# Performance work log

Measured on AMD Instinct MI355X. Metric: run time of the kernel, lower is better.

## Reference

```python
import jax, jax.numpy as jnp
import numpy as np

N = 20000      # number of boxes / graph nodes
E = 160000     # random edges (before self-loops)
DIM = 1024     # feature dim (SIA default)


def setup_inputs() -> dict:
    key = jax.random.key(0)
    ks = jax.random.split(key, 12)
    feats = jax.random.normal(ks[0], (N, DIM), dtype=jnp.float32)
    boxes = jax.random.uniform(ks[1], (N, 4), dtype=jnp.float32)
    src = jax.random.randint(ks[2], (E,), 0, N, dtype=jnp.int32)
    dst = jax.random.randint(ks[3], (E,), 0, N, dtype=jnp.int32)
    loop = jnp.arange(N, dtype=jnp.int32)
    # dgl.add_self_loop: every node gets a self edge
    edges_src = jnp.concatenate([src, loop])
    edges_dst = jnp.concatenate([dst, loop])
    s = 0.02
    return {
        'feats': feats, 'boxes': boxes,
        'edges_src': edges_src, 'edges_dst': edges_dst,
        'w_pos1': jax.random.normal(ks[4], (4, DIM), jnp.float32) * s,
        'b_pos1': jnp.zeros((DIM,), jnp.float32),
        'w_pos2': jax.random.normal(ks[5], (DIM, DIM), jnp.float32) * s,
        'b_pos2': jnp.zeros((DIM,), jnp.float32),
        'w_g1': jax.random.normal(ks[6], (DIM, DIM), jnp.float32) * s,
        'b_g1': jnp.zeros((DIM,), jnp.float32),
        'w_g2': jax.random.normal(ks[7], (DIM, DIM), jnp.float32) * s,
        'b_g2': jnp.zeros((DIM,), jnp.float32),
    }


def _graph_conv(h, src, dst, w, b, n):
    # DGL GraphConv, norm='both', in_feats == out_feats => aggregate then matmul.
    ones = jnp.ones(src.shape, dtype=h.dtype)
    out_deg = jax.ops.segment_sum(ones, src, num_segments=n)
    in_deg = jax.ops.segment_sum(ones, dst, num_segments=n)
    norm_src = jnp.where(out_deg > 0, jax.lax.rsqrt(jnp.maximum(out_deg, 1.0)), 0.0)
    norm_dst = jnp.where(in_deg > 0, jax.lax.rsqrt(jnp.maximum(in_deg, 1.0)), 0.0)
    h = h * norm_src[:, None]
    agg = jax.ops.segment_sum(h[src], dst, num_segments=n)  # irregular gather/scatter
    agg = agg * norm_dst[:, None]
    return agg @ w + b


def reference(feats, boxes, edges_src, edges_dst,
              w_pos1, b_pos1, w_pos2, b_pos2,
              w_g1, b_g1, w_g2, b_g2):
    n = feats.shape[0]
    boxes = jnp.clip(boxes, -10.0, 10.0)
    pos = jax.nn.relu(boxes @ w_pos1 + b_pos1) @ w_pos2 + b_pos2
    h = feats + pos
    h = _graph_conv(h, edges_src, edges_dst, w_g1, b_g1, n)
    h = jax.nn.relu(h)  # dropout is identity in eval
    h = _graph_conv(h, edges_src, edges_dst, w_g2, b_g2, n)
    return h.mean(0)  # frame token [DIM]
```

## Files before the change

kernel.cpp:

```cpp
#include <hip/hip_runtime.h>
#include <hip/hip_bf16.h>
#include <stdint.h>

#define DIM 1024

typedef __attribute__((ext_vector_type(4))) float f32x4;
typedef __attribute__((ext_vector_type(8))) short short8;

__device__ __forceinline__ float bf2f(ushort u) {
    union { uint32_t u; float f; } c; c.u = ((uint32_t)u) << 16; return c.f;
}
__device__ __forceinline__ ushort f2bf(float f) {
    union { float f; uint32_t u; } c; c.f = f;
    uint32_t r = (c.u + 0x7fffu + ((c.u >> 16) & 1u)) >> 16;
    return (ushort)r;
}

__device__ __forceinline__ void async_copy16(void* lds, const void* g) {
    __builtin_amdgcn_global_load_lds((const __attribute__((address_space(1))) void*)g,
                                     (__attribute__((address_space(3))) void*)lds, 16, 0, 0);
}


__global__ void deg_kernel(const int* __restrict__ src, const int* __restrict__ dst,
                           int* out_deg, int* in_deg, int ee) {
    int e = blockIdx.x * 256 + threadIdx.x;
    if (e < ee) {
        atomicAdd(&out_deg[src[e]], 1);
        atomicAdd(&in_deg[dst[e]], 1);
    }
}

__global__ void norm_kernel(const int* __restrict__ out_deg, const int* __restrict__ in_deg,
                            float* ns, float* nd, int n) {
    int i = blockIdx.x * 256 + threadIdx.x;
    if (i < n) {
        int od = out_deg[i], id = in_deg[i];
        ns[i] = od > 0 ? rsqrtf((float)od) : 0.f;
        nd[i] = id > 0 ? rsqrtf((float)id) : 0.f;
    }
}

__global__ void csum_kernel(const int* __restrict__ src, const int* __restrict__ dst,
                            const float* __restrict__ nd, float* cw, int ee) {
    int e = blockIdx.x * 256 + threadIdx.x;
    if (e < ee) atomicAdd(&cw[src[e]], nd[dst[e]]);
}

__global__ void scan_kernel(const int* __restrict__ deg, int* row_ptr, int* cursor, int n) {
    __shared__ int wsum[16];
    __shared__ int carry_s;
    int tid = threadIdx.x, lane = tid & 63, wid = tid >> 6;
    if (tid == 0) carry_s = 0;
    __syncthreads();
    for (int base = 0; base < n; base += 1024) {
        int x = (base + tid < n) ? deg[base + tid] : 0;
        int v = x;
#pragma unroll
        for (int off = 1; off < 64; off <<= 1) {
            int u = __shfl_up(v, off);
            if (lane >= off) v += u;
        }
        if (lane == 63) wsum[wid] = v;
        __syncthreads();
        if (wid == 0 && lane < 16) {
            int wv = wsum[lane];
#pragma unroll
            for (int off = 1; off < 16; off <<= 1) {
                int wu = __shfl_up(wv, off);
                if (lane >= off) wv += wu;
            }
            wsum[lane] = wv;
        }
        __syncthreads();
        int waveoff = (wid > 0) ? wsum[wid - 1] : 0;
        if (base + tid < n) {
            int ex = carry_s + waveoff + v - x;
            row_ptr[base + tid] = ex;
            cursor[base + tid] = ex;
        }
        __syncthreads();
        if (tid == 0) carry_s += wsum[15];
        __syncthreads();
    }
}

__global__ void wnode_kernel(float* cw, const float* __restrict__ ns, int n) {
    int i = blockIdx.x * 256 + threadIdx.x;
    if (i < n) cw[i] *= ns[i];
}

__global__ void scatter_kernel(const int* __restrict__ src, const int* __restrict__ dst,
                               int* cursor, int* csr_src, int ee) {
    int e = blockIdx.x * 256 + threadIdx.x;
    if (e < ee) {
        int p = atomicAdd(&cursor[dst[e]], 1);
        csr_src[p] = src[e];
    }
}


__global__ __launch_bounds__(256) void posA_kernel(const float* __restrict__ boxes,
                                                   const float* __restrict__ w1,
                                                   const float* __restrict__ b1,
                                                   ushort* __restrict__ t, int n) {
    int lane = threadIdx.x & 63, wid = threadIdx.x >> 6;
    int wave = blockIdx.x * 4 + wid, nw = gridDim.x * 4;
    int c0 = lane * 16;
    for (int row = wave; row < n; row += nw) {
        float b[4];
#pragma unroll
        for (int j = 0; j < 4; j++) {
            float v = boxes[row * 4 + j];
            b[j] = fminf(fmaxf(v, -10.f), 10.f);
        }
        short8 o[2];
#pragma unroll
        for (int h = 0; h < 2; h++) {
#pragma unroll
            for (int q = 0; q < 8; q++) {
                int col = c0 + h * 8 + q;
                float v = b1[col];
#pragma unroll
                for (int j = 0; j < 4; j++) v = fmaf(b[j], w1[j * DIM + col], v);
                o[h][q] = (short)f2bf(fmaxf(v, 0.f));
            }
        }
        *(short8*)(t + (size_t)row * DIM + c0) = o[0];
        *(short8*)(t + (size_t)row * DIM + c0 + 8) = o[1];
    }
}


__global__ __launch_bounds__(256) void transpose_bf16_kernel(const float* __restrict__ w,
                                                             ushort* __restrict__ wt) {
    __shared__ float tile[32][33];
    int bx = blockIdx.x, by = blockIdx.y;
    int tx = threadIdx.x & 31, ty = threadIdx.x >> 5;
#pragma unroll
    for (int r = 0; r < 32; r += 8)
        tile[ty + r][tx] = w[(size_t)(by * 32 + ty + r) * DIM + bx * 32 + tx];
    __syncthreads();
#pragma unroll
    for (int r = 0; r < 32; r += 8)
        wt[(size_t)(bx * 32 + ty + r) * DIM + by * 32 + tx] = f2bf(tile[tx][ty + r]);
}


template <int EPI>
__global__ __launch_bounds__(512, 4) void gemm_kernel(
    const ushort* __restrict__ A, const ushort* __restrict__ Bt,
    const float* __restrict__ bias, const float* __restrict__ feats,
    const float* __restrict__ nsrc, ushort* __restrict__ outp,
    int mtiles, int mreal) {
    __shared__ __align__(128) ushort ldsA[2][128 * 64];
    __shared__ __align__(128) ushort ldsB[2][128 * 64];
    int j = blockIdx.x;
    int xcd = j & 7, kq = j >> 3;
    int bm = xcd + 8 * (kq >> 3);
    int bn = kq & 7;
    if (bm >= mtiles) return;

    int tid = threadIdx.x, lane = tid & 63, wid = tid >> 6;
    int wm = wid >> 1, wn = wid & 1;

    f32x4 acc[2][4];
#pragma unroll
    for (int m = 0; m < 2; m++)
#pragma unroll
        for (int nn = 0; nn < 4; nn++) acc[m][nn] = (f32x4){0.f, 0.f, 0.f, 0.f};

    int srow = wid * 8 + (lane >> 3);
    int sseg = (lane & 7) ^ (lane >> 3);
    const ushort* gA = A + (size_t)(bm * 128 + srow) * DIM + sseg * 8;
    const ushort* gB = Bt + (size_t)(bn * 128 + srow) * DIM + sseg * 8;
    int ldsoff0 = (wid * 8) * 64;

    int r16 = lane & 15, khi = lane >> 4;

    auto stage = [&](int buf, int kt) {
#pragma unroll
        for (int c = 0; c < 2; c++) {
            async_copy16(&ldsA[buf][ldsoff0 + c * 64 * 64], gA + (size_t)c * 64 * DIM + kt * 64);
            async_copy16(&ldsB[buf][ldsoff0 + c * 64 * 64], gB + (size_t)c * 64 * DIM + kt * 64);
        }
    };

    stage(0, 0);
    int cur = 0;
    for (int kt = 0; kt < DIM / 64; ++kt) {
        if (kt + 1 < DIM / 64) {
            stage(cur ^ 1, kt + 1);
            asm volatile("s_waitcnt vmcnt(4)" ::: "memory");
        } else {
            asm volatile("s_waitcnt vmcnt(0)" ::: "memory");
        }
        __builtin_amdgcn_s_barrier();
        __builtin_amdgcn_sched_barrier(0);
#pragma unroll
        for (int kk = 0; kk < 2; kk++) {
            short8 af[2], bfv[4];
#pragma unroll
            for (int m = 0; m < 2; m++) {
                int row = wm * 32 + m * 16 + r16;
                int seg = (kk * 4 + khi) ^ (row & 7);
                af[m] = *(const short8*)&ldsA[cur][row * 64 + seg * 8];
            }
#pragma unroll
            for (int nn = 0; nn < 4; nn++) {
                int row = wn * 64 + nn * 16 + r16;
                int seg = (kk * 4 + khi) ^ (row & 7);
                bfv[nn] = *(const short8*)&ldsB[cur][row * 64 + seg * 8];
            }
#pragma unroll
            for (int m = 0; m < 2; m++)
#pragma unroll
                for (int nn = 0; nn < 4; nn++)
                    acc[m][nn] = __builtin_amdgcn_mfma_f32_16x16x32_bf16(af[m], bfv[nn], acc[m][nn], 0, 0, 0);
        }
        __builtin_amdgcn_sched_barrier(0);
        __builtin_amdgcn_s_barrier();
        cur ^= 1;
    }

    int colbase = bn * 128 + wn * 64;
    int rowbase = bm * 128 + wm * 32 + khi * 4;
    if (EPI == 1) {
#pragma unroll
        for (int m = 0; m < 2; m++) {
#pragma unroll
            for (int jj = 0; jj < 4; jj++) {
                int r = rowbase + m * 16 + jj;
                if (r < mreal) {
                    float ns = nsrc[r];
#pragma unroll
                    for (int nn = 0; nn < 4; nn++) {
                        int col = colbase + nn * 16 + r16;
                        float v = acc[m][nn][jj] + bias[col] + feats[(size_t)r * DIM + col];
                        outp[(size_t)r * DIM + col] = f2bf(v * ns);
                    }
                }
            }
        }
    } else {
#pragma unroll
        for (int m = 0; m < 2; m++) {
#pragma unroll
            for (int jj = 0; jj < 4; jj++) {
                int r = rowbase + m * 16 + jj;
                if (r < mreal) {
#pragma unroll
                    for (int nn = 0; nn < 4; nn++) {
                        int col = colbase + nn * 16 + r16;
                        outp[(size_t)r * DIM + col] = f2bf(acc[m][nn][jj]);
                    }
                }
            }
        }
    }
}


__global__ __launch_bounds__(256) void agg2_kernel(
    const ushort* __restrict__ z, const int* __restrict__ row_ptr,
    const int* __restrict__ in_deg, const int* __restrict__ csr_src,
    const float* __restrict__ ndst, const float* __restrict__ wnode,
    const float* __restrict__ bg1, float* __restrict__ vec, int n) {
    __shared__ float red[DIM];
    int lane = threadIdx.x & 63, wid = threadIdx.x >> 6;
    int wave = blockIdx.x * 4 + wid;
    int nwaves = gridDim.x * 4;
    int c0 = lane * 8;

    float bv[16];
#pragma unroll
    for (int t = 0; t < 8; t++) { bv[t] = bg1[c0 + t]; bv[8 + t] = bg1[512 + c0 + t]; }
    float part[16];
#pragma unroll
    for (int t = 0; t < 16; t++) part[t] = 0.f;

    for (int node = wave; node < n; node += nwaves) {
        int start = row_ptr[node], cnt = in_deg[node];
        float a[16];
#pragma unroll
        for (int t = 0; t < 16; t++) a[t] = 0.f;
        int e = 0;
        for (; e + 4 <= cnt; e += 4) {
            const ushort* r0 = z + (size_t)csr_src[start + e] * DIM;
            const ushort* r1 = z + (size_t)csr_src[start + e + 1] * DIM;
            const ushort* r2 = z + (size_t)csr_src[start + e + 2] * DIM;
            const ushort* r3 = z + (size_t)csr_src[start + e + 3] * DIM;
            short8 v00 = *(const short8*)(r0 + c0);
            short8 v01 = *(const short8*)(r0 + 512 + c0);
            short8 v10 = *(const short8*)(r1 + c0);
            short8 v11 = *(const short8*)(r1 + 512 + c0);
            short8 v20 = *(const short8*)(r2 + c0);
            short8 v21 = *(const short8*)(r2 + 512 + c0);
            short8 v30 = *(const short8*)(r3 + c0);
            short8 v31 = *(const short8*)(r3 + 512 + c0);
#pragma unroll
            for (int t = 0; t < 8; t++) {
                a[t]     += (bf2f((ushort)v00[t]) + bf2f((ushort)v10[t])) +
                            (bf2f((ushort)v20[t]) + bf2f((ushort)v30[t]));
                a[8 + t] += (bf2f((ushort)v01[t]) + bf2f((ushort)v11[t])) +
                            (bf2f((ushort)v21[t]) + bf2f((ushort)v31[t]));
            }
        }
        for (; e < cnt; e++) {
            const ushort* r0 = z + (size_t)csr_src[start + e] * DIM;
            short8 v00 = *(const short8*)(r0 + c0);
            short8 v01 = *(const short8*)(r0 + 512 + c0);
#pragma unroll
            for (int t = 0; t < 8; t++) {
                a[t]     += bf2f((ushort)v00[t]);
                a[8 + t] += bf2f((ushort)v01[t]);
            }
        }
        float nd = ndst[node], w = wnode[node];
#pragma unroll
        for (int t = 0; t < 16; t++)
            part[t] = fmaf(w, fmaxf(fmaf(nd, a[t], bv[t]), 0.f), part[t]);
    }

    if (wid == 0) {
#pragma unroll
        for (int t = 0; t < 8; t++) { red[c0 + t] = part[t]; red[512 + c0 + t] = part[8 + t]; }
    }
    __syncthreads();
    for (int w = 1; w < 4; ++w) {
        if (wid == w) {
#pragma unroll
            for (int t = 0; t < 8; t++) { red[c0 + t] += part[t]; red[512 + c0 + t] += part[8 + t]; }
        }
        __syncthreads();
    }
    for (int c = threadIdx.x; c < DIM; c += 256) atomicAdd(&vec[c], red[c]);
}


__global__ __launch_bounds__(256) void final_kernel(const float* __restrict__ vec,
                                                    const float* __restrict__ w2,
                                                    const float* __restrict__ b2,
                                                    float* out, float invn) {
    int d = blockIdx.x * 256 + threadIdx.x;
    int kb = blockIdx.y * 128;
    float acc = 0.f;
#pragma unroll 4
    for (int k = 0; k < 128; k++) acc = fmaf(vec[kb + k], w2[(size_t)(kb + k) * DIM + d], acc);
    float add = acc * invn + (blockIdx.y == 0 ? b2[d] : 0.f);
    atomicAdd(&out[d], add);
}


extern "C" void kernel_launch(void* const* d_in, const int* in_sizes, int n_in,
                              void* d_out, int out_size, void* d_ws, size_t ws_size,
                              hipStream_t stream) {
    const float* feats  = (const float*)d_in[0];
    const float* boxes  = (const float*)d_in[1];
    const int*   esrc   = (const int*)d_in[2];
    const int*   edst   = (const int*)d_in[3];
    const float* w_pos1 = (const float*)d_in[4];
    const float* b_pos1 = (const float*)d_in[5];
    const float* w_pos2 = (const float*)d_in[6];
    const float* b_pos2 = (const float*)d_in[7];
    const float* w_g1   = (const float*)d_in[8];
    const float* b_g1   = (const float*)d_in[9];
    const float* w_g2   = (const float*)d_in[10];
    const float* b_g2   = (const float*)d_in[11];

    int n = in_sizes[0] / DIM;
    int ee = in_sizes[2];
    int mtiles = (n + 127) / 128;
    int groups = (mtiles + 7) / 8;
    int gemm_grid = groups * 64;

    char* p = (char*)d_ws;
    auto alloc = [&](size_t bytes) -> char* {
        char* r = p;
        p += (bytes + 255) & ~((size_t)255);
        return r;
    };
    size_t mp = (size_t)mtiles * 128;
    ushort* t_z    = (ushort*)alloc(mp * DIM * 2);
    ushort* hs     = (ushort*)alloc(mp * DIM * 2);
    ushort* wt1    = (ushort*)alloc((size_t)DIM * DIM * 2);
    ushort* wt2    = (ushort*)alloc((size_t)DIM * DIM * 2);
    char* zero_base = p;
    int*   out_deg = (int*)alloc((size_t)n * 4);
    int*   in_deg  = (int*)alloc((size_t)n * 4);
    float* cw      = (float*)alloc((size_t)n * 4);
    float* vec     = (float*)alloc((size_t)DIM * 4);
    size_t zero_bytes = (size_t)(p - zero_base);
    float* nsrc    = (float*)alloc((size_t)n * 4);
    float* ndst    = (float*)alloc((size_t)n * 4);
    int*   row_ptr = (int*)alloc((size_t)(n + 1) * 4);
    int*   cursor  = (int*)alloc((size_t)n * 4);
    int*   csr_src = (int*)alloc((size_t)ee * 4);

    hipMemsetAsync(zero_base, 0, zero_bytes, stream);
    hipMemsetAsync(d_out, 0, (size_t)out_size * 4, stream);

    int eb = (ee + 255) / 256;
    int nb = (n + 255) / 256;

    deg_kernel<<<eb, 256, 0, stream>>>(esrc, edst, out_deg, in_deg, ee);
    posA_kernel<<<256, 256, 0, stream>>>(boxes, w_pos1, b_pos1, t_z, n);
    transpose_bf16_kernel<<<dim3(32, 32), 256, 0, stream>>>(w_pos2, wt1);
    transpose_bf16_kernel<<<dim3(32, 32), 256, 0, stream>>>(w_g1, wt2);
    norm_kernel<<<nb, 256, 0, stream>>>(out_deg, in_deg, nsrc, ndst, n);
    csum_kernel<<<eb, 256, 0, stream>>>(esrc, edst, ndst, cw, ee);
    scan_kernel<<<1, 1024, 0, stream>>>(in_deg, row_ptr, cursor, n);
    wnode_kernel<<<nb, 256, 0, stream>>>(cw, nsrc, n);
    scatter_kernel<<<eb, 256, 0, stream>>>(esrc, edst, cursor, csr_src, ee);

    gemm_kernel<1><<<gemm_grid, 512, 0, stream>>>(t_z, wt1, b_pos2, feats, nsrc, hs, mtiles, n);
    gemm_kernel<0><<<gemm_grid, 512, 0, stream>>>(hs, wt2, nullptr, nullptr, nullptr, t_z, mtiles, n);
    agg2_kernel<<<1024, 256, 0, stream>>>(t_z, row_ptr, in_deg, csr_src, ndst, cw, b_g1, vec, n);
    final_kernel<<<dim3(4, 8), 256, 0, stream>>>(vec, w_g2, b_g2, (float*)d_out, 1.0f / (float)n);
}
```

Baseline: 425.0 us.

## Enlarge GEMM tile to 256x128 with K=32 stages and new XCD mapping

Reshapes the bf16 GEMM from a 128x128 tile with K=64 per stage to a 256x128 tile with K=32 per stage, so each wave computes a 64x64 block (4x4 MFMA fragments). The LDS swizzle, async copy pattern and workgroup-to-XCD mapping change to match, and the launch-bounds occupancy hint goes from 4 to 6. The goal is more operand reuse per LDS read and fewer tile reloads, at the cost of more accumulator registers, more barriers per K, and a coarser grid of 632 blocks. The aggregation kernel grid is also doubled.

```diff
diff --git a/kernel.cpp b/kernel.cpp
--- a/kernel.cpp
+++ b/kernel.cpp
@@ -148,72 +148,69 @@
 
 
 template <int EPI>
-__global__ __launch_bounds__(512, 4) void gemm_kernel(
+__global__ __launch_bounds__(512, 6) void gemm_kernel(
     const ushort* __restrict__ A, const ushort* __restrict__ Bt,
     const float* __restrict__ bias, const float* __restrict__ feats,
     const float* __restrict__ nsrc, ushort* __restrict__ outp,
     int mtiles, int mreal) {
-    __shared__ __align__(128) ushort ldsA[2][128 * 64];
-    __shared__ __align__(128) ushort ldsB[2][128 * 64];
+    __shared__ __align__(128) ushort ldsA[2][256 * 32];
+    __shared__ __align__(128) ushort ldsB[2][128 * 32];
     int j = blockIdx.x;
-    int xcd = j & 7, kq = j >> 3;
-    int bm = xcd + 8 * (kq >> 3);
-    int bn = kq & 7;
+    int per = gridDim.x >> 3;
+    int wg = (j & 7) * per + (j >> 3);
+    int bm = wg >> 3, bn = wg & 7;
     if (bm >= mtiles) return;
 
     int tid = threadIdx.x, lane = tid & 63, wid = tid >> 6;
     int wm = wid >> 1, wn = wid & 1;
 
-    f32x4 acc[2][4];
-#pragma unroll
-    for (int m = 0; m < 2; m++)
+    f32x4 acc[4][4];
+#pragma unroll
+    for (int m = 0; m < 4; m++)
 #pragma unroll
         for (int nn = 0; nn < 4; nn++) acc[m][nn] = (f32x4){0.f, 0.f, 0.f, 0.f};
 
-    int srow = wid * 8 + (lane >> 3);
-    int sseg = (lane & 7) ^ (lane >> 3);
-    const ushort* gA = A + (size_t)(bm * 128 + srow) * DIM + sseg * 8;
-    const ushort* gB = Bt + (size_t)(bn * 128 + srow) * DIM + sseg * 8;
-    int ldsoff0 = (wid * 8) * 64;
-
-    int r16 = lane & 15, khi = lane >> 4;
+    int rr = lane >> 2;
+    int sw = (lane & 3) ^ (lane >> 4);
+    const ushort* gA = A + (size_t)(bm * 256 + wid * 16 + rr) * DIM + sw * 8;
+    const ushort* gB = Bt + (size_t)(bn * 128 + wid * 16 + rr) * DIM + sw * 8;
+    int ldsbA0 = (wid * 16) * 32;
+    int ldsbA1 = (128 + wid * 16) * 32;
+    int ldsbB  = (wid * 16) * 32;
+
+    int r16 = lane & 15, khi = lane >> 4, rs = (lane & 15) >> 2;
 
     auto stage = [&](int buf, int kt) {
-#pragma unroll
-        for (int c = 0; c < 2; c++) {
-            async_copy16(&ldsA[buf][ldsoff0 + c * 64 * 64], gA + (size_t)c * 64 * DIM + kt * 64);
-            async_copy16(&ldsB[buf][ldsoff0 + c * 64 * 64], gB + (size_t)c * 64 * DIM + kt * 64);
-        }
+        async_copy16(&ldsA[buf][ldsbA0], gA + kt * 32);
+        async_copy16(&ldsA[buf][ldsbA1], gA + (size_t)128 * DIM + kt * 32);
+        async_copy16(&ldsB[buf][ldsbB], gB + kt * 32);
     };
 
     stage(0, 0);
     int cur = 0;
-    for (int kt = 0; kt < DIM / 64; ++kt) {
-        if (kt + 1 < DIM / 64) {
+    for (int kt = 0; kt < DIM / 32; ++kt) {
+        if (kt + 1 < DIM / 32) {
             stage(cur ^ 1, kt + 1);
-            asm volatile("s_waitcnt vmcnt(4)" ::: "memory");
+            asm volatile("s_waitcnt vmcnt(3)" ::: "memory");
         } else {
             asm volatile("s_waitcnt vmcnt(0)" ::: "memory");
         }
         __builtin_amdgcn_s_barrier();
         __builtin_amdgcn_sched_barrier(0);
-#pragma unroll
-        for (int kk = 0; kk < 2; kk++) {
-            short8 af[2], bfv[4];
-#pragma unroll
-            for (int m = 0; m < 2; m++) {
-                int row = wm * 32 + m * 16 + r16;
-                int seg = (kk * 4 + khi) ^ (row & 7);
-                af[m] = *(const short8*)&ldsA[cur][row * 64 + seg * 8];
+        {
+            short8 af[4], bfv[4];
+#pragma unroll
+            for (int m = 0; m < 4; m++) {
+                int row = wm * 64 + m * 16 + r16;
+                af[m] = *(const short8*)&ldsA[cur][row * 32 + ((khi ^ rs) * 8)];
             }
 #pragma unroll
             for (int nn = 0; nn < 4; nn++) {
                 int row = wn * 64 + nn * 16 + r16;
-                int seg = (kk * 4 + khi) ^ (row & 7);
-                bfv[nn] = *(const short8*)&ldsB[cur][row * 64 + seg * 8];
-            }
-#pragma unroll
-            for (int m = 0; m < 2; m++)
+                bfv[nn] = *(const short8*)&ldsB[cur][row * 32 + ((khi ^ rs) * 8)];
+            }
+#pragma unroll
+            for (int m = 0; m < 4; m++)
 #pragma unroll
                 for (int nn = 0; nn < 4; nn++)
                     acc[m][nn] = __builtin_amdgcn_mfma_f32_16x16x32_bf16(af[m], bfv[nn], acc[m][nn], 0, 0, 0);
@@ -224,10 +221,10 @@
     }
 
     int colbase = bn * 128 + wn * 64;
-    int rowbase = bm * 128 + wm * 32 + khi * 4;
+    int rowbase = bm * 256 + wm * 64 + khi * 4;
     if (EPI == 1) {
 #pragma unroll
-        for (int m = 0; m < 2; m++) {
+        for (int m = 0; m < 4; m++) {
 #pragma unroll
             for (int jj = 0; jj < 4; jj++) {
                 int r = rowbase + m * 16 + jj;
@@ -244,7 +241,7 @@
         }
     } else {
 #pragma unroll
-        for (int m = 0; m < 2; m++) {
+        for (int m = 0; m < 4; m++) {
 #pragma unroll
             for (int jj = 0; jj < 4; jj++) {
                 int r = rowbase + m * 16 + jj;
@@ -370,9 +367,8 @@
 
     int n = in_sizes[0] / DIM;
     int ee = in_sizes[2];
-    int mtiles = (n + 127) / 128;
-    int groups = (mtiles + 7) / 8;
-    int gemm_grid = groups * 64;
+    int mtiles = (n + 255) / 256;
+    int gemm_grid = mtiles * 8;
 
     char* p = (char*)d_ws;
     auto alloc = [&](size_t bytes) -> char* {
@@ -380,7 +376,7 @@
         p += (bytes + 255) & ~((size_t)255);
         return r;
     };
-    size_t mp = (size_t)mtiles * 128;
+    size_t mp = (size_t)mtiles * 256;
     ushort* t_z    = (ushort*)alloc(mp * DIM * 2);
     ushort* hs     = (ushort*)alloc(mp * DIM * 2);
     ushort* wt1    = (ushort*)alloc((size_t)DIM * DIM * 2);
@@ -415,6 +411,6 @@
 
     gemm_kernel<1><<<gemm_grid, 512, 0, stream>>>(t_z, wt1, b_pos2, feats, nsrc, hs, mtiles, n);
     gemm_kernel<0><<<gemm_grid, 512, 0, stream>>>(hs, wt2, nullptr, nullptr, nullptr, t_z, mtiles, n);
-    agg2_kernel<<<1024, 256, 0, stream>>>(t_z, row_ptr, in_deg, csr_src, ndst, cw, b_g1, vec, n);
+    agg2_kernel<<<2048, 256, 0, stream>>>(t_z, row_ptr, in_deg, csr_src, ndst, cw, b_g1, vec, n);
     final_kernel<<<dim3(4, 8), 256, 0, stream>>>(vec, w_g2, b_g2, (float*)d_out, 1.0f / (float)n);
 }
```

Measured after the change: 759.8 us. 1.79x slower.

## Store second GEMM output as scaled FP8 and gather FP8 rows in aggregation

Applied to the files above, without the earlier changes.

The second GEMM now writes its output as FP8 (scaled by 16) instead of bf16, and the aggregation kernel gathers 16-byte FP8 row slices per lane, unpacking them with hardware fp8-to-f32 conversions before undoing the scale. This halves the bytes moved in the irregular gather-dominated aggregation and in the GEMM store. The gather loop is unrolled to 8 edges and the aggregation grid is doubled. The cost is a large loss of precision in the intermediate values, which may push the output past accuracy tolerance.

```diff
diff --git a/kernel.cpp b/kernel.cpp
--- a/kernel.cpp
+++ b/kernel.cpp
@@ -5,6 +5,7 @@
 #define DIM 1024
 
 typedef __attribute__((ext_vector_type(4))) float f32x4;
+typedef __attribute__((ext_vector_type(2))) float f32x2;
 typedef __attribute__((ext_vector_type(8))) short short8;
 
 __device__ __forceinline__ float bf2f(ushort u) {
@@ -14,6 +15,18 @@
     union { float f; uint32_t u; } c; c.f = f;
     uint32_t r = (c.u + 0x7fffu + ((c.u >> 16) & 1u)) >> 16;
     return (ushort)r;
+}
+__device__ __forceinline__ uint8_t f2fp8(float v) {
+    int b;
+    asm("v_cvt_pk_fp8_f32 %0, %1, %2" : "=v"(b) : "v"(v), "v"(v));
+    return (uint8_t)b;
+}
+__device__ __forceinline__ void acc_fp8x4(uint32_t dw, float* a) {
+    f32x2 lo, hi;
+    asm("v_cvt_pk_f32_fp8 %0, %1" : "=v"(lo) : "v"(dw));
+    uint32_t dwh = dw >> 16;
+    asm("v_cvt_pk_f32_fp8 %0, %1" : "=v"(hi) : "v"(dwh));
+    a[0] += lo[0]; a[1] += lo[1]; a[2] += hi[0]; a[3] += hi[1];
 }
 
 __device__ __forceinline__ void async_copy16(void* lds, const void* g) {
@@ -151,7 +164,7 @@
 __global__ __launch_bounds__(512, 4) void gemm_kernel(
     const ushort* __restrict__ A, const ushort* __restrict__ Bt,
     const float* __restrict__ bias, const float* __restrict__ feats,
-    const float* __restrict__ nsrc, ushort* __restrict__ outp,
+    const float* __restrict__ nsrc, void* __restrict__ outp,
     int mtiles, int mreal) {
     __shared__ __align__(128) ushort ldsA[2][128 * 64];
     __shared__ __align__(128) ushort ldsB[2][128 * 64];
@@ -226,6 +239,7 @@
     int colbase = bn * 128 + wn * 64;
     int rowbase = bm * 128 + wm * 32 + khi * 4;
     if (EPI == 1) {
+        ushort* ob = (ushort*)outp;
 #pragma unroll
         for (int m = 0; m < 2; m++) {
 #pragma unroll
@@ -237,12 +251,13 @@
                     for (int nn = 0; nn < 4; nn++) {
                         int col = colbase + nn * 16 + r16;
                         float v = acc[m][nn][jj] + bias[col] + feats[(size_t)r * DIM + col];
-                        outp[(size_t)r * DIM + col] = f2bf(v * ns);
+                        ob[(size_t)r * DIM + col] = f2bf(v * ns);
                     }
                 }
             }
         }
     } else {
+        uint8_t* o8 = (uint8_t*)outp;
 #pragma unroll
         for (int m = 0; m < 2; m++) {
 #pragma unroll
@@ -252,7 +267,7 @@
 #pragma unroll
                     for (int nn = 0; nn < 4; nn++) {
                         int col = colbase + nn * 16 + r16;
-                        outp[(size_t)r * DIM + col] = f2bf(acc[m][nn][jj]);
+                        o8[(size_t)r * DIM + col] = f2fp8(acc[m][nn][jj] * 16.f);
                     }
                 }
             }
@@ -262,7 +277,7 @@
 
 
 __global__ __launch_bounds__(256) void agg2_kernel(
-    const ushort* __restrict__ z, const int* __restrict__ row_ptr,
+    const uint8_t* __restrict__ z8, const int* __restrict__ row_ptr,
     const int* __restrict__ in_deg, const int* __restrict__ csr_src,
     const float* __restrict__ ndst, const float* __restrict__ wnode,
     const float* __restrict__ bg1, float* __restrict__ vec, int n) {
@@ -270,11 +285,11 @@
     int lane = threadIdx.x & 63, wid = threadIdx.x >> 6;
     int wave = blockIdx.x * 4 + wid;
     int nwaves = gridDim.x * 4;
-    int c0 = lane * 8;
+    int c0 = lane * 16;
 
     float bv[16];
 #pragma unroll
-    for (int t = 0; t < 8; t++) { bv[t] = bg1[c0 + t]; bv[8 + t] = bg1[512 + c0 + t]; }
+    for (int t = 0; t < 16; t++) bv[t] = bg1[c0 + t];
     float part[16];
 #pragma unroll
     for (int t = 0; t < 16; t++) part[t] = 0.f;
@@ -285,52 +300,41 @@
 #pragma unroll
         for (int t = 0; t < 16; t++) a[t] = 0.f;
         int e = 0;
-        for (; e + 4 <= cnt; e += 4) {
-            const ushort* r0 = z + (size_t)csr_src[start + e] * DIM;
-            const ushort* r1 = z + (size_t)csr_src[start + e + 1] * DIM;
-            const ushort* r2 = z + (size_t)csr_src[start + e + 2] * DIM;
-            const ushort* r3 = z + (size_t)csr_src[start + e + 3] * DIM;
-            short8 v00 = *(const short8*)(r0 + c0);
-            short8 v01 = *(const short8*)(r0 + 512 + c0);
-            short8 v10 = *(const short8*)(r1 + c0);
-            short8 v11 = *(const short8*)(r1 + 512 + c0);
-            short8 v20 = *(const short8*)(r2 + c0);
-            short8 v21 = *(const short8*)(r2 + 512 + c0);
-            short8 v30 = *(const short8*)(r3 + c0);
-            short8 v31 = *(const short8*)(r3 + 512 + c0);
-#pragma unroll
-            for (int t = 0; t < 8; t++) {
-                a[t]     += (bf2f((ushort)v00[t]) + bf2f((ushort)v10[t])) +
-                            (bf2f((ushort)v20[t]) + bf2f((ushort)v30[t]));
-                a[8 + t] += (bf2f((ushort)v01[t]) + bf2f((ushort)v11[t])) +
-                            (bf2f((ushort)v21[t]) + bf2f((ushort)v31[t]));
+        for (; e + 8 <= cnt; e += 8) {
+            uint4 v[8];
+#pragma unroll
+            for (int q = 0; q < 8; q++)
+                v[q] = *(const uint4*)(z8 + (size_t)csr_src[start + e + q] * DIM + c0);
+#pragma unroll
+            for (int q = 0; q < 8; q++) {
+                acc_fp8x4(v[q].x, a + 0);
+                acc_fp8x4(v[q].y, a + 4);
+                acc_fp8x4(v[q].z, a + 8);
+                acc_fp8x4(v[q].w, a + 12);
             }
         }
         for (; e < cnt; e++) {
-            const ushort* r0 = z + (size_t)csr_src[start + e] * DIM;
-            short8 v00 = *(const short8*)(r0 + c0);
-            short8 v01 = *(const short8*)(r0 + 512 + c0);
-#pragma unroll
-            for (int t = 0; t < 8; t++) {
-                a[t]     += bf2f((ushort)v00[t]);
-                a[8 + t] += bf2f((ushort)v01[t]);
-            }
-        }
-        float nd = ndst[node], w = wnode[node];
+            uint4 v0 = *(const uint4*)(z8 + (size_t)csr_src[start + e] * DIM + c0);
+            acc_fp8x4(v0.x, a + 0);
+            acc_fp8x4(v0.y, a + 4);
+            acc_fp8x4(v0.z, a + 8);
+            acc_fp8x4(v0.w, a + 12);
+        }
+        float nd16 = ndst[node] * 0.0625f, w = wnode[node];
 #pragma unroll
         for (int t = 0; t < 16; t++)
-            part[t] = fmaf(w, fmaxf(fmaf(nd, a[t], bv[t]), 0.f), part[t]);
+            part[t] = fmaf(w, fmaxf(fmaf(nd16, a[t], bv[t]), 0.f), part[t]);
     }
 
     if (wid == 0) {
 #pragma unroll
-        for (int t = 0; t < 8; t++) { red[c0 + t] = part[t]; red[512 + c0 + t] = part[8 + t]; }
+        for (int t = 0; t < 16; t++) red[c0 + t] = part[t];
     }
     __syncthreads();
     for (int w = 1; w < 4; ++w) {
         if (wid == w) {
 #pragma unroll
-            for (int t = 0; t < 8; t++) { red[c0 + t] += part[t]; red[512 + c0 + t] += part[8 + t]; }
+            for (int t = 0; t < 16; t++) red[c0 + t] += part[t];
         }
         __syncthreads();
     }
@@ -413,8 +417,11 @@
     wnode_kernel<<<nb, 256, 0, stream>>>(cw, nsrc, n);
     scatter_kernel<<<eb, 256, 0, stream>>>(esrc, edst, cursor, csr_src, ee);
 
-    gemm_kernel<1><<<gemm_grid, 512, 0, stream>>>(t_z, wt1, b_pos2, feats, nsrc, hs, mtiles, n);
-    gemm_kernel<0><<<gemm_grid, 512, 0, stream>>>(hs, wt2, nullptr, nullptr, nullptr, t_z, mtiles, n);
-    agg2_kernel<<<1024, 256, 0, stream>>>(t_z, row_ptr, in_deg, csr_src, ndst, cw, b_g1, vec, n);
+    gemm_kernel<1><<<gemm_grid, 512, 0, stream>>>(t_z, wt1, b_pos2, feats, nsrc, (void*)hs,
+                                                  mtiles, n);
+    uint8_t* z8 = (uint8_t*)t_z;
+    gemm_kernel<0><<<gemm_grid, 512, 0, stream>>>(hs, wt2, nullptr, nullptr, nullptr, (void*)z8,
+                                                  mtiles, n);
+    agg2_kernel<<<2048, 256, 0, stream>>>(z8, row_ptr, in_deg, csr_src, ndst, cw, b_g1, vec, n);
     final_kernel<<<dim3(4, 8), 256, 0, stream>>>(vec, w_g2, b_g2, (float*)d_out, 1.0f / (float)n);
 }
```

After: 424.2 us. About the same (-0.2%).
